# Kernel optimization log

Hardware: AMD Instinct MI355X
Metric: run time of the kernel (lower is better)

## Reference

```python
import jax, jax.numpy as jnp
import numpy as np

N = 262144          # total atoms
B = 2048            # graphs (batch.max()+1)
HID = 256           # hidden
CND = 128           # cond_proj_dim
K = 16              # n_clusters
PH = 8              # pool_heads
DH = HID // PH      # head_dim


def setup_inputs() -> dict:
    key = jax.random.key(0)
    ks = jax.random.split(key, 20)
    s = 0.02
    inp = {
        "h_atom": jax.random.normal(ks[0], (N, HID), jnp.float32),
        "c_atom": jax.random.normal(ks[1], (N, CND), jnp.float32),
        "batch": jnp.sort(jax.random.randint(ks[2], (N,), 0, B)).astype(jnp.int64),
        # gate: Linear(HID+CND, HID) -> GELU -> Linear(HID, 1) -> Sigmoid
        "W1": jax.random.normal(ks[3], (HID + CND, HID), jnp.float32) * s,
        "b1": jnp.zeros((HID,), jnp.float32),
        "W2": jax.random.normal(ks[4], (HID, 1), jnp.float32) * s,
        "b2": jnp.zeros((1,), jnp.float32),
        # assign: Linear(HID, HID) -> GELU -> Linear(HID, K)
        "A1": jax.random.normal(ks[5], (HID, HID), jnp.float32) * s,
        "ab1": jnp.zeros((HID,), jnp.float32),
        "A2": jax.random.normal(ks[6], (HID, K), jnp.float32) * s,
        "ab2": jnp.zeros((K,), jnp.float32),
        # cluster_proj: Linear(HID, HID)
        "Wc": jax.random.normal(ks[7], (HID, HID), jnp.float32) * s,
        "bc": jnp.zeros((HID,), jnp.float32),
        # readout
        "q": jax.random.normal(ks[8], (PH, DH), jnp.float32),   # readout_q param
        "Wk": jax.random.normal(ks[9], (HID, HID), jnp.float32) * s,
        "Wv": jax.random.normal(ks[10], (HID, HID), jnp.float32) * s,
        # LayerNorm
        "gamma": jnp.ones((HID,), jnp.float32),
        "beta": jnp.zeros((HID,), jnp.float32),
    }
    return inp


def reference(h_atom, c_atom, batch, W1, b1, W2, b2, A1, ab1, A2, ab2,
              Wc, bc, q, Wk, Wv, gamma, beta):
    gelu = lambda x: jax.nn.gelu(x, approximate=False)  # torch default GELU (erf)
    # Stage 1: condition-aware gating
    g = gelu(jnp.concatenate([h_atom, c_atom], axis=-1) @ W1 + b1)
    alpha = jax.nn.sigmoid(g @ W2 + b2)                 # [N, 1]
    h_gated = alpha * h_atom                            # [N, HID]
    # Stage 2: soft cluster assignment
    S = jax.nn.softmax(gelu(h_gated @ A1 + ab1) @ A2 + ab2, axis=-1)  # [N, K]
    # Ragged per-graph segment matmul: cluster[b,k,:] = sum_{n in graph b} S[n,k] * h_gated[n,:]
    cluster = jnp.stack(
        [jax.ops.segment_sum(h_gated * S[:, k:k + 1], batch, num_segments=B)
         for k in range(K)], axis=1)                    # [B, K, HID]
    cluster = cluster @ Wc + bc                         # cluster_proj
    # Stage 3: multi-head attention readout over K clusters
    Kp = (cluster @ Wk).reshape(B, K, PH, DH)
    Vp = (cluster @ Wv).reshape(B, K, PH, DH)
    scale = DH ** -0.5
    logits = jnp.einsum('pd,bkpd->bpk', q, Kp) * scale  # [B, PH, K]
    w = jax.nn.softmax(logits, axis=-1)                 # dropout p=0 -> identity
    out = jnp.einsum('bpk,bkpd->bpd', w, Vp).reshape(B, HID)
    # LayerNorm (eps = 1e-5, torch default)
    mu = out.mean(axis=-1, keepdims=True)
    var = ((out - mu) ** 2).mean(axis=-1, keepdims=True)
    return (out - mu) * jax.lax.rsqrt(var + 1e-5) * gamma + beta
```

## Files before the change

### kernel.cpp

```cpp
#include <hip/hip_runtime.h>
#include <hip/hip_bf16.h>
#include <math.h>
#include <stdint.h>

#define NATOMS 262144
#define BGRAPH 2048
#define CHUNK 10240

typedef __bf16 bf16_t;
typedef __bf16 bf16x8 __attribute__((ext_vector_type(8)));
typedef __bf16 bf16x4 __attribute__((ext_vector_type(4)));
typedef float f32x4 __attribute__((ext_vector_type(4)));

__device__ __forceinline__ float bf2f(bf16_t x){ return (float)x; }
__device__ __forceinline__ float gelu_f(float x){ return 0.5f*x*(1.0f+erff(x*0.70710678118654752f)); }

__device__ __forceinline__ void gl_lds16(const void* g, void* l){
    __attribute__((address_space(3))) uint32_t* lp =
        reinterpret_cast<__attribute__((address_space(3))) uint32_t*>(
            reinterpret_cast<uintptr_t>(l));
    __builtin_amdgcn_global_load_lds(static_cast<const uint32_t*>(g), lp, 16, 0, 0);
}

__global__ void bounds_kernel(const int* __restrict__ batch,
                              const unsigned* __restrict__ gamma,
                              int* __restrict__ starts, int* __restrict__ flags) {
    if (blockIdx.x == 0 && threadIdx.x == 0)
        flags[0] = (gamma[0] == 0x3F803F80u) ? 1 : 0;
    int b = blockIdx.x * 256 + threadIdx.x;
    if (b > BGRAPH) return;
    int is64 = (batch[NATOMS - 1] == 0) ? 1 : 0;
    int lo = 0, hi = NATOMS;
    while (lo < hi) {
        int mid = (lo + hi) >> 1;
        int v = is64 ? batch[2 * mid] : batch[mid];
        if (v < b) lo = mid + 1; else hi = mid;
    }
    starts[b] = lo;
}

__global__ void params_kernel(const void* b1, const void* W2, const void* ab1,
                              const void* bc, const void* q, const void* gamma,
                              const void* beta, const void* ab2, const void* b2,
                              float* __restrict__ P, const int* __restrict__ flags) {
    int t = threadIdx.x;
    int bf = flags[0];
#define CV(p,i) (bf ? bf2f(((const bf16_t*)(p))[i]) : ((const float*)(p))[i])
    P[t]        = CV(b1, t);
    P[256 + t]  = CV(W2, t);
    P[512 + t]  = CV(ab1, t);
    P[768 + t]  = CV(bc, t);
    P[1024 + t] = CV(q, t);
    P[1280 + t] = CV(gamma, t);
    P[1536 + t] = CV(beta, t);
    if (t < 16) P[1792 + t] = CV(ab2, t);
    if (t == 16) P[1808] = CV(b2, 0);
#undef CV
}

__global__ void chunk_transpose(const void* __restrict__ src, bf16_t* __restrict__ dst,
                                int Kd, int Nn, const int* __restrict__ flags) {
    int i = blockIdx.x * 256 + threadIdx.x;
    if (i >= Kd * Nn) return;
    int k = i / Nn, n = i - k * Nn;
    bf16_t v = flags[0] ? ((const bf16_t*)src)[i] : (bf16_t)(((const float*)src)[i]);
    dst[((size_t)(k >> 5) * Nn + n) * 40 + (k & 31)] = v;
}

__global__ void a2_transpose(const void* __restrict__ src, bf16_t* __restrict__ dst,
                             const int* __restrict__ flags) {
    int i = blockIdx.x * 256 + threadIdx.x;
    if (i >= 256 * 16) return;
    int k = i >> 4, n = i & 15;
    bf16_t v = flags[0] ? ((const bf16_t*)src)[i] : (bf16_t)(((const float*)src)[i]);
    dst[n * 256 + k] = v;
}

__global__ void c_convert(const float* __restrict__ c, bf16_t* __restrict__ cb,
                          const int* __restrict__ flags) {
    if (flags[0]) return;
    const size_t total = (size_t)NATOMS * 128 / 8;
    for (size_t i = (size_t)blockIdx.x * 256 + threadIdx.x; i < total; i += (size_t)2048 * 256) {
        const float4* s = (const float4*)c + i * 2;
        float4 a = s[0], b = s[1];
        bf16x8 v = { (bf16_t)a.x,(bf16_t)a.y,(bf16_t)a.z,(bf16_t)a.w,
                     (bf16_t)b.x,(bf16_t)b.y,(bf16_t)b.z,(bf16_t)b.w };
        *(bf16x8*)(cb + i * 8) = v;
    }
}

__global__ __launch_bounds__(256, 2) void atom_kernel(
    const void* __restrict__ h, const void* __restrict__ cnd, const bf16_t* __restrict__ cb,
    const bf16_t* __restrict__ W1c, const bf16_t* __restrict__ A1c,
    const bf16_t* __restrict__ A2t, const float* __restrict__ P,
    const int* __restrict__ flags,
    bf16_t* __restrict__ hg_out, float* __restrict__ S_out)
{
    __shared__ bf16_t ldsX[64 * 264];
    __shared__ bf16_t ldsW[2][CHUNK];
    __shared__ float  ldsV[256];
    __shared__ float  ldsB1[256];
    __shared__ float  ldsAB1[256];
    __shared__ float  ldsAlpha[64];

    const int tid  = threadIdx.x;
    const int wave = tid >> 6;
    const int lane = tid & 63;
    const int quad = lane >> 4;
    const int l15  = lane & 15;
    const int a0   = blockIdx.x * 64;
    const int dbf  = flags[0];

    const bf16_t* cbp = dbf ? (const bf16_t*)cnd : cb;

    bf16x8 cf[4][4];
#pragma unroll
    for (int kc = 0; kc < 4; ++kc)
#pragma unroll
        for (int mt = 0; mt < 4; ++mt)
            cf[kc][mt] = *(const bf16x8*)(cbp + (size_t)(a0 + mt * 16 + l15) * 128 + kc * 32 + quad * 8);

    ldsV[tid]   = P[256 + tid];
    ldsB1[tid]  = P[tid];
    ldsAB1[tid] = P[512 + tid];
    if (tid < 64) ldsAlpha[tid] = 0.f;
    const float b2v = P[1808];

    if (dbf) {
        const uint4* hs = (const uint4*)((const bf16_t*)h + (size_t)a0 * 256);
#pragma unroll
        for (int i = 0; i < 8; ++i) {
            int lin = i * 256 + tid; int row = lin >> 5; int off = lin & 31;
            *(uint4*)(&ldsX[row * 264 + off * 8]) = hs[row * 32 + off];
        }
    } else {
        const float4* hs = (const float4*)((const float*)h + (size_t)a0 * 256);
#pragma unroll
        for (int i = 0; i < 16; ++i) {
            int lin = i * 256 + tid; int row = lin >> 6; int off = lin & 63;
            float4 v = hs[row * 64 + off];
            bf16x4 w = { (bf16_t)v.x, (bf16_t)v.y, (bf16_t)v.z, (bf16_t)v.w };
            *(bf16x4*)(&ldsX[row * 264 + off * 4]) = w;
        }
    }

    auto stage = [&](int bsel, const bf16_t* src){
#pragma unroll
        for (int i = 0; i < 5; ++i) {
            int u = i * 256 + wave * 64;
            gl_lds16(src + (size_t)(u + lane) * 8, &ldsW[bsel][u * 8]);
        }
    };

    stage(0, W1c);
    __syncthreads();

    f32x4 acc[4][4];
#pragma unroll
    for (int a = 0; a < 4; ++a)
#pragma unroll
        for (int b = 0; b < 4; ++b) acc[a][b] = (f32x4){0.f,0.f,0.f,0.f};

#pragma unroll
    for (int ks = 0; ks < 12; ++ks) {
        const int cur = ks & 1;
        const bf16_t* nxt = (ks < 11) ? (W1c + (size_t)(ks + 1) * CHUNK) : A1c;
        stage(cur ^ 1, nxt);
        bf16x8 af[4], bv[4];
#pragma unroll
        for (int j = 0; j < 4; ++j)
            bv[j] = *(const bf16x8*)(&ldsW[cur][(wave * 64 + j * 16 + l15) * 40 + quad * 8]);
        if (ks < 8) {
            int kb = ks * 32 + quad * 8;
#pragma unroll
            for (int mt = 0; mt < 4; ++mt) af[mt] = *(const bf16x8*)(&ldsX[(mt * 16 + l15) * 264 + kb]);
        } else {
#pragma unroll
            for (int mt = 0; mt < 4; ++mt) af[mt] = cf[ks - 8][mt];
        }
        __builtin_amdgcn_s_setprio(1);
#pragma unroll
        for (int mt = 0; mt < 4; ++mt)
#pragma unroll
            for (int j = 0; j < 4; ++j)
                acc[mt][j] = __builtin_amdgcn_mfma_f32_16x16x32_bf16(af[mt], bv[j], acc[mt][j], 0, 0, 0);
        __builtin_amdgcn_s_setprio(0);
        __syncthreads();
    }

    for (int mt = 0; mt < 4; ++mt) {
        float p[4] = {0.f, 0.f, 0.f, 0.f};
        for (int j = 0; j < 4; ++j) {
            int col = wave * 64 + j * 16 + l15;
            float w = ldsV[col];
            float bb = ldsB1[col];
            for (int r = 0; r < 4; ++r) {
                float g = gelu_f(acc[mt][j][r] + bb);
                p[r] += g * w;
            }
        }
        for (int off = 1; off < 16; off <<= 1)
            for (int r = 0; r < 4; ++r) p[r] += __shfl_xor(p[r], off, 64);
        if (l15 == 0)
            for (int r = 0; r < 4; ++r)
                atomicAdd(&ldsAlpha[mt * 16 + quad * 4 + r], p[r]);
    }
    __syncthreads();

    {
        int r = tid >> 2, p4 = tid & 3;
        float al = 1.f / (1.f + expf(-(ldsAlpha[r] + b2v)));
        bf16_t* xrow = &ldsX[r * 264 + p4 * 64];
        bf16_t* grow = hg_out + (size_t)(a0 + r) * 256 + p4 * 64;
        for (int i = 0; i < 8; ++i) {
            bf16x8 v = *(bf16x8*)(xrow + i * 8);
            for (int e = 0; e < 8; ++e) v[e] = (bf16_t)(bf2f(v[e]) * al);
            *(bf16x8*)(xrow + i * 8) = v;
            *(bf16x8*)(grow + i * 8) = v;
        }
    }
    __syncthreads();

#pragma unroll
    for (int a = 0; a < 4; ++a)
#pragma unroll
        for (int b = 0; b < 4; ++b) acc[a][b] = (f32x4){0.f,0.f,0.f,0.f};
#pragma unroll
    for (int ks = 0; ks < 8; ++ks) {
        const int cur = ks & 1;
        if (ks < 7) stage(cur ^ 1, A1c + (size_t)(ks + 1) * CHUNK);
        bf16x8 af[4], bv[4];
        int kb = ks * 32 + quad * 8;
#pragma unroll
        for (int j = 0; j < 4; ++j)
            bv[j] = *(const bf16x8*)(&ldsW[cur][(wave * 64 + j * 16 + l15) * 40 + quad * 8]);
#pragma unroll
        for (int mt = 0; mt < 4; ++mt) af[mt] = *(const bf16x8*)(&ldsX[(mt * 16 + l15) * 264 + kb]);
        __builtin_amdgcn_s_setprio(1);
#pragma unroll
        for (int mt = 0; mt < 4; ++mt)
#pragma unroll
            for (int j = 0; j < 4; ++j)
                acc[mt][j] = __builtin_amdgcn_mfma_f32_16x16x32_bf16(af[mt], bv[j], acc[mt][j], 0, 0, 0);
        __builtin_amdgcn_s_setprio(0);
        __syncthreads();
    }

    for (int mt = 0; mt < 4; ++mt)
        for (int j = 0; j < 4; ++j) {
            int col = wave * 64 + j * 16 + l15;
            float bb = ldsAB1[col];
            for (int r = 0; r < 4; ++r) {
                int row = mt * 16 + quad * 4 + r;
                ldsX[row * 264 + col] = (bf16_t)gelu_f(acc[mt][j][r] + bb);
            }
        }
    if (tid < 128) {
        int n = tid >> 3, k0 = (tid & 7) * 32;
#pragma unroll
        for (int p = 0; p < 4; ++p)
            *(uint4*)(&ldsW[0][n * 264 + k0 + p * 8]) = *(const uint4*)(A2t + n * 256 + k0 + p * 8);
    }
    __syncthreads();

    f32x4 acc3 = (f32x4){0.f,0.f,0.f,0.f};
#pragma unroll
    for (int ks = 0; ks < 8; ++ks) {
        int kb = ks * 32 + quad * 8;
        bf16x8 a = *(const bf16x8*)(&ldsX[(wave * 16 + l15) * 264 + kb]);
        bf16x8 b = *(const bf16x8*)(&ldsW[0][l15 * 264 + kb]);
        acc3 = __builtin_amdgcn_mfma_f32_16x16x32_bf16(a, b, acc3, 0, 0, 0);
    }
    float ab2v = P[1792 + l15];
    float lv[4], mx[4], ex[4], sm[4];
    for (int r = 0; r < 4; ++r) { lv[r] = acc3[r] + ab2v; mx[r] = lv[r]; }
    for (int off = 1; off < 16; off <<= 1)
        for (int r = 0; r < 4; ++r) { float o = __shfl_xor(mx[r], off, 64); mx[r] = fmaxf(mx[r], o); }
    for (int r = 0; r < 4; ++r) { ex[r] = expf(lv[r] - mx[r]); sm[r] = ex[r]; }
    for (int off = 1; off < 16; off <<= 1)
        for (int r = 0; r < 4; ++r) sm[r] += __shfl_xor(sm[r], off, 64);
    for (int r = 0; r < 4; ++r) {
        int row = wave * 16 + quad * 4 + r;
        S_out[(size_t)(a0 + row) * 16 + l15] = ex[r] / sm[r];
    }
}

__global__ __launch_bounds__(256) void segment_kernel(
    const bf16_t* __restrict__ hg, const float* __restrict__ S,
    const int* __restrict__ starts, bf16_t* __restrict__ craw)
{
    __shared__ float ldsS[16 * 16];
    int b = blockIdx.x, tid = threadIdx.x;
    int s = starts[b], e = starts[b + 1];
    float acc[16];
#pragma unroll
    for (int k = 0; k < 16; ++k) acc[k] = 0.f;
    for (int n0 = s; n0 < e; n0 += 16) {
        int cnt = min(16, e - n0);
        if (tid < cnt * 16) ldsS[tid] = S[(size_t)(n0 + (tid >> 4)) * 16 + (tid & 15)];
        __syncthreads();
        for (int a = 0; a < cnt; ++a) {
            float v = bf2f(hg[(size_t)(n0 + a) * 256 + tid]);
            const f32x4* sr = (const f32x4*)(&ldsS[a * 16]);
            f32x4 s0 = sr[0], s1 = sr[1], s2 = sr[2], s3 = sr[3];
            acc[0]  += s0[0] * v; acc[1]  += s0[1] * v; acc[2]  += s0[2] * v; acc[3]  += s0[3] * v;
            acc[4]  += s1[0] * v; acc[5]  += s1[1] * v; acc[6]  += s1[2] * v; acc[7]  += s1[3] * v;
            acc[8]  += s2[0] * v; acc[9]  += s2[1] * v; acc[10] += s2[2] * v; acc[11] += s2[3] * v;
            acc[12] += s3[0] * v; acc[13] += s3[1] * v; acc[14] += s3[2] * v; acc[15] += s3[3] * v;
        }
        __syncthreads();
    }
#pragma unroll
    for (int k = 0; k < 16; ++k)
        craw[((size_t)b * 16 + k) * 256 + tid] = (bf16_t)acc[k];
}

__global__ __launch_bounds__(256, 2) void gemm_kernel(
    const bf16_t* __restrict__ A, const bf16_t* __restrict__ Wck,
    const float* __restrict__ bias, bf16_t* __restrict__ C)
{
    __shared__ bf16_t ldsA[64 * 264];
    __shared__ bf16_t ldsW[2][CHUNK];
    const int tid = threadIdx.x;
    const int wave = tid >> 6, lane = tid & 63, quad = lane >> 4, l15 = lane & 15;
    const size_t r0 = (size_t)blockIdx.x * 64;

    auto stage = [&](int bsel, const bf16_t* src){
#pragma unroll
        for (int i = 0; i < 5; ++i) {
            int u = i * 256 + wave * 64;
            gl_lds16(src + (size_t)(u + lane) * 8, &ldsW[bsel][u * 8]);
        }
    };

    const uint4* as = (const uint4*)(A + r0 * 256);
#pragma unroll
    for (int i = 0; i < 8; ++i) {
        int lin = i * 256 + tid; int row = lin >> 5; int off = lin & 31;
        *(uint4*)(&ldsA[row * 264 + off * 8]) = as[row * 32 + off];
    }
    stage(0, Wck);
    __syncthreads();

    f32x4 acc[4][4];
#pragma unroll
    for (int a = 0; a < 4; ++a)
#pragma unroll
        for (int b = 0; b < 4; ++b) acc[a][b] = (f32x4){0.f,0.f,0.f,0.f};

#pragma unroll
    for (int ks = 0; ks < 8; ++ks) {
        const int cur = ks & 1;
        if (ks < 7) stage(cur ^ 1, Wck + (size_t)(ks + 1) * CHUNK);
        bf16x8 af[4], bv[4];
        int kb = ks * 32 + quad * 8;
#pragma unroll
        for (int j = 0; j < 4; ++j)
            bv[j] = *(const bf16x8*)(&ldsW[cur][(wave * 64 + j * 16 + l15) * 40 + quad * 8]);
#pragma unroll
        for (int mt = 0; mt < 4; ++mt) af[mt] = *(const bf16x8*)(&ldsA[(mt * 16 + l15) * 264 + kb]);
        __builtin_amdgcn_s_setprio(1);
#pragma unroll
        for (int mt = 0; mt < 4; ++mt)
#pragma unroll
            for (int j = 0; j < 4; ++j)
                acc[mt][j] = __builtin_amdgcn_mfma_f32_16x16x32_bf16(af[mt], bv[j], acc[mt][j], 0, 0, 0);
        __builtin_amdgcn_s_setprio(0);
        __syncthreads();
    }
    for (int mt = 0; mt < 4; ++mt)
        for (int j = 0; j < 4; ++j) {
            int col = wave * 64 + j * 16 + l15;
            float bvl = bias ? bias[col] : 0.f;
            for (int r = 0; r < 4; ++r)
                C[(r0 + mt * 16 + quad * 4 + r) * 256 + col] = (bf16_t)(acc[mt][j][r] + bvl);
        }
}

__global__ __launch_bounds__(256, 2) void gemm2x_kernel(
    const bf16_t* __restrict__ A, const bf16_t* __restrict__ Wkc, const bf16_t* __restrict__ Wvc,
    bf16_t* __restrict__ CK, bf16_t* __restrict__ CV)
{
    __shared__ bf16_t ldsA[64 * 264];
    __shared__ bf16_t ldsW[2][CHUNK];
    const int tid = threadIdx.x;
    const int wave = tid >> 6, lane = tid & 63, quad = lane >> 4, l15 = lane & 15;
    const size_t r0 = (size_t)blockIdx.x * 64;

    auto stage = [&](int bsel, const bf16_t* src){
#pragma unroll
        for (int i = 0; i < 5; ++i) {
            int u = i * 256 + wave * 64;
            gl_lds16(src + (size_t)(u + lane) * 8, &ldsW[bsel][u * 8]);
        }
    };

    const uint4* as = (const uint4*)(A + r0 * 256);
#pragma unroll
    for (int i = 0; i < 8; ++i) {
        int lin = i * 256 + tid; int row = lin >> 5; int off = lin & 31;
        *(uint4*)(&ldsA[row * 264 + off * 8]) = as[row * 32 + off];
    }
    stage(0, Wkc);
    __syncthreads();

    f32x4 acc[4][4];
#pragma unroll
    for (int a = 0; a < 4; ++a)
#pragma unroll
        for (int b = 0; b < 4; ++b) acc[a][b] = (f32x4){0.f,0.f,0.f,0.f};

#pragma unroll
    for (int ks = 0; ks < 8; ++ks) {
        const int cur = ks & 1;
        const bf16_t* nxt = (ks < 7) ? (Wkc + (size_t)(ks + 1) * CHUNK) : Wvc;
        stage(cur ^ 1, nxt);
        bf16x8 af[4], bv[4];
        int kb = ks * 32 + quad * 8;
#pragma unroll
        for (int j = 0; j < 4; ++j)
            bv[j] = *(const bf16x8*)(&ldsW[cur][(wave * 64 + j * 16 + l15) * 40 + quad * 8]);
#pragma unroll
        for (int mt = 0; mt < 4; ++mt) af[mt] = *(const bf16x8*)(&ldsA[(mt * 16 + l15) * 264 + kb]);
        __builtin_amdgcn_s_setprio(1);
#pragma unroll
        for (int mt = 0; mt < 4; ++mt)
#pragma unroll
            for (int j = 0; j < 4; ++j)
                acc[mt][j] = __builtin_amdgcn_mfma_f32_16x16x32_bf16(af[mt], bv[j], acc[mt][j], 0, 0, 0);
        __builtin_amdgcn_s_setprio(0);
        __syncthreads();
    }
    for (int mt = 0; mt < 4; ++mt)
        for (int j = 0; j < 4; ++j) {
            int col = wave * 64 + j * 16 + l15;
            for (int r = 0; r < 4; ++r)
                CK[(r0 + mt * 16 + quad * 4 + r) * 256 + col] = (bf16_t)acc[mt][j][r];
        }

#pragma unroll
    for (int a = 0; a < 4; ++a)
#pragma unroll
        for (int b = 0; b < 4; ++b) acc[a][b] = (f32x4){0.f,0.f,0.f,0.f};
#pragma unroll
    for (int ks = 0; ks < 8; ++ks) {
        const int cur = ks & 1;
        if (ks < 7) stage(cur ^ 1, Wvc + (size_t)(ks + 1) * CHUNK);
        bf16x8 af[4], bv[4];
        int kb = ks * 32 + quad * 8;
#pragma unroll
        for (int j = 0; j < 4; ++j)
            bv[j] = *(const bf16x8*)(&ldsW[cur][(wave * 64 + j * 16 + l15) * 40 + quad * 8]);
#pragma unroll
        for (int mt = 0; mt < 4; ++mt) af[mt] = *(const bf16x8*)(&ldsA[(mt * 16 + l15) * 264 + kb]);
        __builtin_amdgcn_s_setprio(1);
#pragma unroll
        for (int mt = 0; mt < 4; ++mt)
#pragma unroll
            for (int j = 0; j < 4; ++j)
                acc[mt][j] = __builtin_amdgcn_mfma_f32_16x16x32_bf16(af[mt], bv[j], acc[mt][j], 0, 0, 0);
        __builtin_amdgcn_s_setprio(0);
        __syncthreads();
    }
    for (int mt = 0; mt < 4; ++mt)
        for (int j = 0; j < 4; ++j) {
            int col = wave * 64 + j * 16 + l15;
            for (int r = 0; r < 4; ++r)
                CV[(r0 + mt * 16 + quad * 4 + r) * 256 + col] = (bf16_t)acc[mt][j][r];
        }
}

__global__ __launch_bounds__(256) void attn_ln_kernel(
    const bf16_t* __restrict__ Kp, const bf16_t* __restrict__ Vp,
    const float* __restrict__ P, const int* __restrict__ flags,
    void* __restrict__ out)
{
    __shared__ float lw[8][16];
    __shared__ float w1s[4], w2s[4];
    int b = blockIdx.x, tid = threadIdx.x;
    const int dbf = flags[0];
    const float* q     = P + 1024;
    const float* gamma = P + 1280;
    const float* beta  = P + 1536;
    if (tid < 128) {
        int p = tid >> 4, k = tid & 15;
        const bf16x8* kr = (const bf16x8*)(Kp + ((size_t)b * 16 + k) * 256 + p * 32);
        const float* qr = q + p * 32;
        float dot = 0.f;
#pragma unroll
        for (int i = 0; i < 4; ++i) {
            bf16x8 v = kr[i];
#pragma unroll
            for (int e = 0; e < 8; ++e) dot += qr[i * 8 + e] * bf2f(v[e]);
        }
        lw[p][k] = dot * 0.17677669529663687f;
    }
    __syncthreads();
    if (tid < 8) {
        float m = -1e30f;
        for (int k = 0; k < 16; ++k) m = fmaxf(m, lw[tid][k]);
        float s = 0.f;
        for (int k = 0; k < 16; ++k) { float ev = expf(lw[tid][k] - m); lw[tid][k] = ev; s += ev; }
        float inv = 1.f / s;
        for (int k = 0; k < 16; ++k) lw[tid][k] *= inv;
    }
    __syncthreads();
    int p = tid >> 5, d = tid & 31;
    float o = 0.f;
    for (int k = 0; k < 16; ++k)
        o += lw[p][k] * bf2f(Vp[((size_t)b * 16 + k) * 256 + p * 32 + d]);
    float s1 = o, s2 = o * o;
    for (int off = 1; off < 64; off <<= 1) { s1 += __shfl_xor(s1, off, 64); s2 += __shfl_xor(s2, off, 64); }
    int wv = tid >> 6;
    if ((tid & 63) == 0) { w1s[wv] = s1; w2s[wv] = s2; }
    __syncthreads();
    float ts1 = w1s[0] + w1s[1] + w1s[2] + w1s[3];
    float ts2 = w2s[0] + w2s[1] + w2s[2] + w2s[3];
    float mu = ts1 * (1.f / 256.f);
    float var = ts2 * (1.f / 256.f) - mu * mu;
    float y = (o - mu) * rsqrtf(var + 1e-5f) * gamma[tid] + beta[tid];
    if (dbf) ((bf16_t*)out)[(size_t)b * 256 + tid] = (bf16_t)y;
    else     ((float*)out)[(size_t)b * 256 + tid]  = y;
}

extern "C" void kernel_launch(void* const* d_in, const int* in_sizes, int n_in,
                              void* d_out, int out_size, void* d_ws, size_t ws_size,
                              hipStream_t stream) {
    const void* h     = d_in[0];
    const void* cnd   = d_in[1];
    const int*  batch = (const int*)d_in[2];
    const void* W1    = d_in[3];
    const void* b1    = d_in[4];
    const void* W2    = d_in[5];
    const void* b2    = d_in[6];
    const void* A1    = d_in[7];
    const void* ab1   = d_in[8];
    const void* A2    = d_in[9];
    const void* ab2   = d_in[10];
    const void* Wc    = d_in[11];
    const void* bc    = d_in[12];
    const void* q     = d_in[13];
    const void* Wk    = d_in[14];
    const void* Wv    = d_in[15];
    const void* gamma = d_in[16];
    const void* beta  = d_in[17];

    char* ws = (char*)d_ws;
    size_t off = 0;
    bf16_t* W1c  = (bf16_t*)(ws + off); off += 12 * CHUNK * 2;
    bf16_t* A1c  = (bf16_t*)(ws + off); off += 8 * CHUNK * 2;
    bf16_t* Wcc  = (bf16_t*)(ws + off); off += 8 * CHUNK * 2;
    bf16_t* Wkc  = (bf16_t*)(ws + off); off += 8 * CHUNK * 2;
    bf16_t* Wvc  = (bf16_t*)(ws + off); off += 8 * CHUNK * 2;
    bf16_t* A2t  = (bf16_t*)(ws + off); off += 8192;
    float*  P    = (float*)(ws + off);  off += 8192;
    int*    flags = (int*)(ws + off);   off += 256;
    int*    starts = (int*)(ws + off);  off += 8448;
    float*  S    = (float*)(ws + off);  off += (size_t)NATOMS * 16 * 4;
    bf16_t* hg   = (bf16_t*)(ws + off); off += (size_t)NATOMS * 256 * 2;
    bf16_t* craw = (bf16_t*)(ws + off); off += (size_t)BGRAPH * 16 * 256 * 2;
    bf16_t* cP   = (bf16_t*)(ws + off); off += (size_t)BGRAPH * 16 * 256 * 2;
    bf16_t* KpB  = (bf16_t*)(ws + off); off += (size_t)BGRAPH * 16 * 256 * 2;
    bf16_t* VpB  = (bf16_t*)(ws + off); off += (size_t)BGRAPH * 16 * 256 * 2;
    bf16_t* cb   = craw;
    (void)ws_size; (void)n_in; (void)in_sizes; (void)out_size;

    bounds_kernel<<<9, 256, 0, stream>>>(batch, (const unsigned*)gamma, starts, flags);
    params_kernel<<<1, 256, 0, stream>>>(b1, W2, ab1, bc, q, gamma, beta, ab2, b2, P, flags);
    chunk_transpose<<<(384 * 256 + 255) / 256, 256, 0, stream>>>(W1, W1c, 384, 256, flags);
    chunk_transpose<<<(256 * 256 + 255) / 256, 256, 0, stream>>>(A1, A1c, 256, 256, flags);
    chunk_transpose<<<(256 * 256 + 255) / 256, 256, 0, stream>>>(Wc, Wcc, 256, 256, flags);
    chunk_transpose<<<(256 * 256 + 255) / 256, 256, 0, stream>>>(Wk, Wkc, 256, 256, flags);
    chunk_transpose<<<(256 * 256 + 255) / 256, 256, 0, stream>>>(Wv, Wvc, 256, 256, flags);
    a2_transpose<<<16, 256, 0, stream>>>(A2, A2t, flags);
    c_convert<<<2048, 256, 0, stream>>>((const float*)cnd, cb, flags);

    atom_kernel<<<NATOMS / 64, 256, 0, stream>>>(h, cnd, cb, W1c, A1c, A2t, P, flags, hg, S);
    segment_kernel<<<BGRAPH, 256, 0, stream>>>(hg, S, starts, craw);
    gemm_kernel<<<BGRAPH * 16 / 64, 256, 0, stream>>>(craw, Wcc, P + 768, cP);
    gemm2x_kernel<<<BGRAPH * 16 / 64, 256, 0, stream>>>(cP, Wkc, Wvc, KpB, VpB);
    attn_ln_kernel<<<BGRAPH, 256, 0, stream>>>(KpB, VpB, P, flags, d_out);
}
```

Before: 835.9 us.

## Merge prep kernels, fuse cluster GEMMs, enlarge atom tiles, use fast GELU/exp

Nine small setup launches are merged into one prep kernel that dispatches on block index. The cluster_proj GEMM and the K/V GEMM are fused, so the projected cluster stays in LDS instead of round-tripping through global memory. The atom kernel now runs 128 atoms per 512-thread block with 64-wide K steps, which halves the barrier count per unit of work and shares weight staging across twice as many rows, but it roughly doubles LDS per block and may lower occupancy. erf in GELU is replaced by the Abramowitz-Stegun polynomial, and exp and reciprocal use fast intrinsics, trading a little accuracy for fewer instructions.

Measured after the change: 807.6 us. 3.4% less time.

```diff
diff --git a/kernel.cpp b/kernel.cpp
--- a/kernel.cpp
+++ b/kernel.cpp
@@ -13,7 +13,17 @@
 typedef float f32x4 __attribute__((ext_vector_type(4)));
 
 __device__ __forceinline__ float bf2f(bf16_t x){ return (float)x; }
-__device__ __forceinline__ float gelu_f(float x){ return 0.5f*x*(1.0f+erff(x*0.70710678118654752f)); }
+
+__device__ __forceinline__ float gelu_f(float x){
+    float s  = x * 0.70710678118654752f;
+    float a  = fabsf(s);
+    float t  = __builtin_amdgcn_rcpf(fmaf(0.3275911f, a, 1.0f));
+    float p  = t * fmaf(t, fmaf(t, fmaf(t, fmaf(t, 1.061405429f, -1.453152027f),
+                                        1.421413741f), -0.284496736f), 0.254829592f);
+    float e  = __expf(-a * a);
+    float er = copysignf(fmaf(-p, e, 1.0f), s);
+    return 0.5f * x * (1.0f + er);
+}
 
 __device__ __forceinline__ void gl_lds16(const void* g, void* l){
     __attribute__((address_space(3))) uint32_t* lp =
@@ -22,93 +32,113 @@
     __builtin_amdgcn_global_load_lds(static_cast<const uint32_t*>(g), lp, 16, 0, 0);
 }
 
-__global__ void bounds_kernel(const int* __restrict__ batch,
-                              const unsigned* __restrict__ gamma,
-                              int* __restrict__ starts, int* __restrict__ flags) {
-    if (blockIdx.x == 0 && threadIdx.x == 0)
-        flags[0] = (gamma[0] == 0x3F803F80u) ? 1 : 0;
-    int b = blockIdx.x * 256 + threadIdx.x;
-    if (b > BGRAPH) return;
-    int is64 = (batch[NATOMS - 1] == 0) ? 1 : 0;
-    int lo = 0, hi = NATOMS;
-    while (lo < hi) {
-        int mid = (lo + hi) >> 1;
-        int v = is64 ? batch[2 * mid] : batch[mid];
-        if (v < b) lo = mid + 1; else hi = mid;
-    }
-    starts[b] = lo;
-}
-
-__global__ void params_kernel(const void* b1, const void* W2, const void* ab1,
-                              const void* bc, const void* q, const void* gamma,
-                              const void* beta, const void* ab2, const void* b2,
-                              float* __restrict__ P, const int* __restrict__ flags) {
-    int t = threadIdx.x;
-    int bf = flags[0];
+#define PREP_W1 10
+#define PREP_A1 394
+#define PREP_WC 650
+#define PREP_WK 906
+#define PREP_WV 1162
+#define PREP_A2 1418
+#define PREP_C  1434
+#define PREP_END 3482
+
+__device__ __forceinline__ void chunk_tr(const void* src, bf16_t* dst, int Kd, int idx, int bf){
+    if (idx >= Kd * 256) return;
+    int k = idx >> 8, n = idx & 255;
+    bf16_t v = bf ? ((const bf16_t*)src)[idx] : (bf16_t)(((const float*)src)[idx]);
+    dst[((size_t)(k >> 5) * 256 + n) * 40 + (k & 31)] = v;
+}
+
+__global__ void prep_kernel(
+    const int* __restrict__ batch, const void* __restrict__ gamma,
+    const void* b1, const void* W2, const void* ab1, const void* bc,
+    const void* q, const void* beta, const void* ab2, const void* b2,
+    const void* W1, const void* A1, const void* Wc, const void* Wk, const void* Wv,
+    const void* A2, const void* cnd,
+    bf16_t* __restrict__ W1c, bf16_t* __restrict__ A1c, bf16_t* __restrict__ Wcc,
+    bf16_t* __restrict__ Wkc, bf16_t* __restrict__ Wvc, bf16_t* __restrict__ A2t,
+    float* __restrict__ P, int* __restrict__ flags, int* __restrict__ starts,
+    bf16_t* __restrict__ cbOut)
+{
+    const int tid = threadIdx.x, blk = blockIdx.x;
+    const int bf = (((const unsigned*)gamma)[0] == 0x3F803F80u) ? 1 : 0;
+    if (blk == 0 && tid == 0) flags[0] = bf;
+
+    if (blk < 9) {
+        int b = blk * 256 + tid;
+        if (b > BGRAPH) return;
+        int is64 = (batch[NATOMS - 1] == 0) ? 1 : 0;
+        int lo = 0, hi = NATOMS;
+        while (lo < hi) {
+            int mid = (lo + hi) >> 1;
+            int v = is64 ? batch[2 * mid] : batch[mid];
+            if (v < b) lo = mid + 1; else hi = mid;
+        }
+        starts[b] = lo;
+        return;
+    }
+    if (blk == 9) {
 #define CV(p,i) (bf ? bf2f(((const bf16_t*)(p))[i]) : ((const float*)(p))[i])
-    P[t]        = CV(b1, t);
-    P[256 + t]  = CV(W2, t);
-    P[512 + t]  = CV(ab1, t);
-    P[768 + t]  = CV(bc, t);
-    P[1024 + t] = CV(q, t);
-    P[1280 + t] = CV(gamma, t);
-    P[1536 + t] = CV(beta, t);
-    if (t < 16) P[1792 + t] = CV(ab2, t);
-    if (t == 16) P[1808] = CV(b2, 0);
+        P[tid]        = CV(b1, tid);
+        P[256 + tid]  = CV(W2, tid);
+        P[512 + tid]  = CV(ab1, tid);
+        P[768 + tid]  = CV(bc, tid);
+        P[1024 + tid] = CV(q, tid);
+        P[1280 + tid] = CV(gamma, tid);
+        P[1536 + tid] = CV(beta, tid);
+        if (tid < 16) P[1792 + tid] = CV(ab2, tid);
+        if (tid == 16) P[1808] = CV(b2, 0);
 #undef CV
-}
-
-__global__ void chunk_transpose(const void* __restrict__ src, bf16_t* __restrict__ dst,
-                                int Kd, int Nn, const int* __restrict__ flags) {
-    int i = blockIdx.x * 256 + threadIdx.x;
-    if (i >= Kd * Nn) return;
-    int k = i / Nn, n = i - k * Nn;
-    bf16_t v = flags[0] ? ((const bf16_t*)src)[i] : (bf16_t)(((const float*)src)[i]);
-    dst[((size_t)(k >> 5) * Nn + n) * 40 + (k & 31)] = v;
-}
-
-__global__ void a2_transpose(const void* __restrict__ src, bf16_t* __restrict__ dst,
-                             const int* __restrict__ flags) {
-    int i = blockIdx.x * 256 + threadIdx.x;
-    if (i >= 256 * 16) return;
-    int k = i >> 4, n = i & 15;
-    bf16_t v = flags[0] ? ((const bf16_t*)src)[i] : (bf16_t)(((const float*)src)[i]);
-    dst[n * 256 + k] = v;
-}
-
-__global__ void c_convert(const float* __restrict__ c, bf16_t* __restrict__ cb,
-                          const int* __restrict__ flags) {
-    if (flags[0]) return;
+        return;
+    }
+    if (blk < PREP_A1) { chunk_tr(W1, W1c, 384, (blk - PREP_W1) * 256 + tid, bf); return; }
+    if (blk < PREP_WC) { chunk_tr(A1, A1c, 256, (blk - PREP_A1) * 256 + tid, bf); return; }
+    if (blk < PREP_WK) { chunk_tr(Wc, Wcc, 256, (blk - PREP_WC) * 256 + tid, bf); return; }
+    if (blk < PREP_WV) { chunk_tr(Wk, Wkc, 256, (blk - PREP_WK) * 256 + tid, bf); return; }
+    if (blk < PREP_A2) { chunk_tr(Wv, Wvc, 256, (blk - PREP_WV) * 256 + tid, bf); return; }
+    if (blk < PREP_C)  {
+        int i = (blk - PREP_A2) * 256 + tid;
+        if (i >= 256 * 16) return;
+        int k = i >> 4, n = i & 15;
+        bf16_t v = bf ? ((const bf16_t*)A2)[i] : (bf16_t)(((const float*)A2)[i]);
+        A2t[n * 256 + k] = v;
+        return;
+    }
+    if (bf) return;
+    size_t i = (size_t)(blk - PREP_C) * 256 + tid;
     const size_t total = (size_t)NATOMS * 128 / 8;
-    for (size_t i = (size_t)blockIdx.x * 256 + threadIdx.x; i < total; i += (size_t)2048 * 256) {
-        const float4* s = (const float4*)c + i * 2;
+#pragma unroll
+    for (int it = 0; it < 8; ++it, i += 524288) {
+        if (i >= total) break;
+        const float4* s = (const float4*)cnd + i * 2;
         float4 a = s[0], b = s[1];
         bf16x8 v = { (bf16_t)a.x,(bf16_t)a.y,(bf16_t)a.z,(bf16_t)a.w,
                      (bf16_t)b.x,(bf16_t)b.y,(bf16_t)b.z,(bf16_t)b.w };
-        *(bf16x8*)(cb + i * 8) = v;
-    }
-}
-
-__global__ __launch_bounds__(256, 2) void atom_kernel(
+        *(bf16x8*)(cbOut + i * 8) = v;
+    }
+}
+
+__global__ __launch_bounds__(512, 2) void atom_kernel(
     const void* __restrict__ h, const void* __restrict__ cnd, const bf16_t* __restrict__ cb,
     const bf16_t* __restrict__ W1c, const bf16_t* __restrict__ A1c,
     const bf16_t* __restrict__ A2t, const float* __restrict__ P,
     const int* __restrict__ flags,
     bf16_t* __restrict__ hg_out, float* __restrict__ S_out)
 {
-    __shared__ bf16_t ldsX[64 * 264];
-    __shared__ bf16_t ldsW[2][CHUNK];
+    __shared__ bf16_t ldsX[128 * 264];
+    __shared__ bf16_t ldsW[2][2 * CHUNK];
     __shared__ float  ldsV[256];
     __shared__ float  ldsB1[256];
     __shared__ float  ldsAB1[256];
-    __shared__ float  ldsAlpha[64];
+    __shared__ float  ldsAlpha[128];
 
     const int tid  = threadIdx.x;
     const int wave = tid >> 6;
     const int lane = tid & 63;
     const int quad = lane >> 4;
     const int l15  = lane & 15;
-    const int a0   = blockIdx.x * 64;
+    const int wr   = wave >> 2;
+    const int wc   = wave & 3;
+    const int a0   = blockIdx.x * 128;
     const int dbf  = flags[0];
 
     const bf16_t* cbp = dbf ? (const bf16_t*)cnd : cb;
@@ -118,26 +148,24 @@
     for (int kc = 0; kc < 4; ++kc)
 #pragma unroll
         for (int mt = 0; mt < 4; ++mt)
-            cf[kc][mt] = *(const bf16x8*)(cbp + (size_t)(a0 + mt * 16 + l15) * 128 + kc * 32 + quad * 8);
-
-    ldsV[tid]   = P[256 + tid];
-    ldsB1[tid]  = P[tid];
-    ldsAB1[tid] = P[512 + tid];
-    if (tid < 64) ldsAlpha[tid] = 0.f;
+            cf[kc][mt] = *(const bf16x8*)(cbp + (size_t)(a0 + wr * 64 + mt * 16 + l15) * 128 + kc * 32 + quad * 8);
+
+    if (tid < 256) { ldsV[tid] = P[256 + tid]; ldsB1[tid] = P[tid]; ldsAB1[tid] = P[512 + tid]; }
+    if (tid < 128) ldsAlpha[tid] = 0.f;
     const float b2v = P[1808];
 
     if (dbf) {
         const uint4* hs = (const uint4*)((const bf16_t*)h + (size_t)a0 * 256);
 #pragma unroll
         for (int i = 0; i < 8; ++i) {
-            int lin = i * 256 + tid; int row = lin >> 5; int off = lin & 31;
+            int lin = i * 512 + tid; int row = lin >> 5; int off = lin & 31;
             *(uint4*)(&ldsX[row * 264 + off * 8]) = hs[row * 32 + off];
         }
     } else {
         const float4* hs = (const float4*)((const float*)h + (size_t)a0 * 256);
 #pragma unroll
         for (int i = 0; i < 16; ++i) {
-            int lin = i * 256 + tid; int row = lin >> 6; int off = lin & 63;
+            int lin = i * 512 + tid; int row = lin >> 6; int off = lin & 63;
             float4 v = hs[row * 64 + off];
             bf16x4 w = { (bf16_t)v.x, (bf16_t)v.y, (bf16_t)v.z, (bf16_t)v.w };
             *(bf16x4*)(&ldsX[row * 264 + off * 4]) = w;
@@ -147,8 +175,8 @@
     auto stage = [&](int bsel, const bf16_t* src){
 #pragma unroll
         for (int i = 0; i < 5; ++i) {
-            int u = i * 256 + wave * 64;
-            gl_lds16(src + (size_t)(u + lane) * 8, &ldsW[bsel][u * 8]);
+            int u = i * 512 + wave * 64;
+            gl_lds16(src + (size_t)(u + lane) * 8, &ldsW[bsel][0] + (size_t)u * 8);
         }
     };
 
@@ -162,28 +190,37 @@
         for (int b = 0; b < 4; ++b) acc[a][b] = (f32x4){0.f,0.f,0.f,0.f};
 
 #pragma unroll
-    for (int ks = 0; ks < 12; ++ks) {
+    for (int ks = 0; ks < 6; ++ks) {
         const int cur = ks & 1;
-        const bf16_t* nxt = (ks < 11) ? (W1c + (size_t)(ks + 1) * CHUNK) : A1c;
+        const bf16_t* nxt = (ks < 5) ? (W1c + (size_t)(ks + 1) * 2 * CHUNK) : A1c;
         stage(cur ^ 1, nxt);
-        bf16x8 af[4], bv[4];
-#pragma unroll
-        for (int j = 0; j < 4; ++j)
-            bv[j] = *(const bf16x8*)(&ldsW[cur][(wave * 64 + j * 16 + l15) * 40 + quad * 8]);
-        if (ks < 8) {
-            int kb = ks * 32 + quad * 8;
-#pragma unroll
-            for (int mt = 0; mt < 4; ++mt) af[mt] = *(const bf16x8*)(&ldsX[(mt * 16 + l15) * 264 + kb]);
+        bf16x8 af[2][4], bv[2][4];
+#pragma unroll
+        for (int kh = 0; kh < 2; ++kh)
+#pragma unroll
+            for (int j = 0; j < 4; ++j)
+                bv[kh][j] = *(const bf16x8*)(&ldsW[cur][kh * CHUNK + (wc * 64 + j * 16 + l15) * 40 + quad * 8]);
+        if (ks < 4) {
+#pragma unroll
+            for (int kh = 0; kh < 2; ++kh)
+#pragma unroll
+                for (int mt = 0; mt < 4; ++mt)
+                    af[kh][mt] = *(const bf16x8*)(&ldsX[(wr * 64 + mt * 16 + l15) * 264 + ks * 64 + kh * 32 + quad * 8]);
         } else {
 #pragma unroll
-            for (int mt = 0; mt < 4; ++mt) af[mt] = cf[ks - 8][mt];
+            for (int kh = 0; kh < 2; ++kh)
+#pragma unroll
+                for (int mt = 0; mt < 4; ++mt)
+                    af[kh][mt] = cf[(ks - 4) * 2 + kh][mt];
         }
         __builtin_amdgcn_s_setprio(1);
 #pragma unroll
-        for (int mt = 0; mt < 4; ++mt)
-#pragma unroll
-            for (int j = 0; j < 4; ++j)
-                acc[mt][j] = __builtin_amdgcn_mfma_f32_16x16x32_bf16(af[mt], bv[j], acc[mt][j], 0, 0, 0);
+        for (int kh = 0; kh < 2; ++kh)
+#pragma unroll
+            for (int mt = 0; mt < 4; ++mt)
+#pragma unroll
+                for (int j = 0; j < 4; ++j)
+                    acc[mt][j] = __builtin_amdgcn_mfma_f32_16x16x32_bf16(af[kh][mt], bv[kh][j], acc[mt][j], 0, 0, 0);
         __builtin_amdgcn_s_setprio(0);
         __syncthreads();
     }
@@ -191,7 +228,7 @@
     for (int mt = 0; mt < 4; ++mt) {
         float p[4] = {0.f, 0.f, 0.f, 0.f};
         for (int j = 0; j < 4; ++j) {
-            int col = wave * 64 + j * 16 + l15;
+            int col = wc * 64 + j * 16 + l15;
             float w = ldsV[col];
             float bb = ldsB1[col];
             for (int r = 0; r < 4; ++r) {
@@ -203,13 +240,13 @@
             for (int r = 0; r < 4; ++r) p[r] += __shfl_xor(p[r], off, 64);
         if (l15 == 0)
             for (int r = 0; r < 4; ++r)
-                atomicAdd(&ldsAlpha[mt * 16 + quad * 4 + r], p[r]);
+                atomicAdd(&ldsAlpha[wr * 64 + mt * 16 + quad * 4 + r], p[r]);
     }
     __syncthreads();
 
     {
         int r = tid >> 2, p4 = tid & 3;
-        float al = 1.f / (1.f + expf(-(ldsAlpha[r] + b2v)));
+        float al = __builtin_amdgcn_rcpf(1.f + __expf(-(ldsAlpha[r] + b2v)));
         bf16_t* xrow = &ldsX[r * 264 + p4 * 64];
         bf16_t* grow = hg_out + (size_t)(a0 + r) * 256 + p4 * 64;
         for (int i = 0; i < 8; ++i) {
@@ -226,32 +263,37 @@
 #pragma unroll
         for (int b = 0; b < 4; ++b) acc[a][b] = (f32x4){0.f,0.f,0.f,0.f};
 #pragma unroll
-    for (int ks = 0; ks < 8; ++ks) {
+    for (int ks = 0; ks < 4; ++ks) {
         const int cur = ks & 1;
-        if (ks < 7) stage(cur ^ 1, A1c + (size_t)(ks + 1) * CHUNK);
-        bf16x8 af[4], bv[4];
-        int kb = ks * 32 + quad * 8;
-#pragma unroll
-        for (int j = 0; j < 4; ++j)
-            bv[j] = *(const bf16x8*)(&ldsW[cur][(wave * 64 + j * 16 + l15) * 40 + quad * 8]);
-#pragma unroll
-        for (int mt = 0; mt < 4; ++mt) af[mt] = *(const bf16x8*)(&ldsX[(mt * 16 + l15) * 264 + kb]);
+        if (ks < 3) stage(cur ^ 1, A1c + (size_t)(ks + 1) * 2 * CHUNK);
+        bf16x8 af[2][4], bv[2][4];
+#pragma unroll
+        for (int kh = 0; kh < 2; ++kh) {
+#pragma unroll
+            for (int j = 0; j < 4; ++j)
+                bv[kh][j] = *(const bf16x8*)(&ldsW[cur][kh * CHUNK + (wc * 64 + j * 16 + l15) * 40 + quad * 8]);
+#pragma unroll
+            for (int mt = 0; mt < 4; ++mt)
+                af[kh][mt] = *(const bf16x8*)(&ldsX[(wr * 64 + mt * 16 + l15) * 264 + ks * 64 + kh * 32 + quad * 8]);
+        }
         __builtin_amdgcn_s_setprio(1);
 #pragma unroll
-        for (int mt = 0; mt < 4; ++mt)
-#pragma unroll
-            for (int j = 0; j < 4; ++j)
-                acc[mt][j] = __builtin_amdgcn_mfma_f32_16x16x32_bf16(af[mt], bv[j], acc[mt][j], 0, 0, 0);
+        for (int kh = 0; kh < 2; ++kh)
+#pragma unroll
+            for (int mt = 0; mt < 4; ++mt)
+#pragma unroll
+                for (int j = 0; j < 4; ++j)
+                    acc[mt][j] = __builtin_amdgcn_mfma_f32_16x16x32_bf16(af[kh][mt], bv[kh][j], acc[mt][j], 0, 0, 0);
         __builtin_amdgcn_s_setprio(0);
         __syncthreads();
     }
 
     for (int mt = 0; mt < 4; ++mt)
         for (int j = 0; j < 4; ++j) {
-            int col = wave * 64 + j * 16 + l15;
+            int col = wc * 64 + j * 16 + l15;
             float bb = ldsAB1[col];
             for (int r = 0; r < 4; ++r) {
-                int row = mt * 16 + quad * 4 + r;
+                int row = wr * 64 + mt * 16 + quad * 4 + r;
                 ldsX[row * 264 + col] = (bf16_t)gelu_f(acc[mt][j][r] + bb);
             }
         }
@@ -276,7 +318,7 @@
     for (int r = 0; r < 4; ++r) { lv[r] = acc3[r] + ab2v; mx[r] = lv[r]; }
     for (int off = 1; off < 16; off <<= 1)
         for (int r = 0; r < 4; ++r) { float o = __shfl_xor(mx[r], off, 64); mx[r] = fmaxf(mx[r], o); }
-    for (int r = 0; r < 4; ++r) { ex[r] = expf(lv[r] - mx[r]); sm[r] = ex[r]; }
+    for (int r = 0; r < 4; ++r) { ex[r] = __expf(lv[r] - mx[r]); sm[r] = ex[r]; }
     for (int off = 1; off < 16; off <<= 1)
         for (int r = 0; r < 4; ++r) sm[r] += __shfl_xor(sm[r], off, 64);
     for (int r = 0; r < 4; ++r) {
@@ -315,70 +357,10 @@
         craw[((size_t)b * 16 + k) * 256 + tid] = (bf16_t)acc[k];
 }
 
-__global__ __launch_bounds__(256, 2) void gemm_kernel(
-    const bf16_t* __restrict__ A, const bf16_t* __restrict__ Wck,
-    const float* __restrict__ bias, bf16_t* __restrict__ C)
-{
-    __shared__ bf16_t ldsA[64 * 264];
-    __shared__ bf16_t ldsW[2][CHUNK];
-    const int tid = threadIdx.x;
-    const int wave = tid >> 6, lane = tid & 63, quad = lane >> 4, l15 = lane & 15;
-    const size_t r0 = (size_t)blockIdx.x * 64;
-
-    auto stage = [&](int bsel, const bf16_t* src){
-#pragma unroll
-        for (int i = 0; i < 5; ++i) {
-            int u = i * 256 + wave * 64;
-            gl_lds16(src + (size_t)(u + lane) * 8, &ldsW[bsel][u * 8]);
-        }
-    };
-
-    const uint4* as = (const uint4*)(A + r0 * 256);
-#pragma unroll
-    for (int i = 0; i < 8; ++i) {
-        int lin = i * 256 + tid; int row = lin >> 5; int off = lin & 31;
-        *(uint4*)(&ldsA[row * 264 + off * 8]) = as[row * 32 + off];
-    }
-    stage(0, Wck);
-    __syncthreads();
-
-    f32x4 acc[4][4];
-#pragma unroll
-    for (int a = 0; a < 4; ++a)
-#pragma unroll
-        for (int b = 0; b < 4; ++b) acc[a][b] = (f32x4){0.f,0.f,0.f,0.f};
-
-#pragma unroll
-    for (int ks = 0; ks < 8; ++ks) {
-        const int cur = ks & 1;
-        if (ks < 7) stage(cur ^ 1, Wck + (size_t)(ks + 1) * CHUNK);
-        bf16x8 af[4], bv[4];
-        int kb = ks * 32 + quad * 8;
-#pragma unroll
-        for (int j = 0; j < 4; ++j)
-            bv[j] = *(const bf16x8*)(&ldsW[cur][(wave * 64 + j * 16 + l15) * 40 + quad * 8]);
-#pragma unroll
-        for (int mt = 0; mt < 4; ++mt) af[mt] = *(const bf16x8*)(&ldsA[(mt * 16 + l15) * 264 + kb]);
-        __builtin_amdgcn_s_setprio(1);
-#pragma unroll
-        for (int mt = 0; mt < 4; ++mt)
-#pragma unroll
-            for (int j = 0; j < 4; ++j)
-                acc[mt][j] = __builtin_amdgcn_mfma_f32_16x16x32_bf16(af[mt], bv[j], acc[mt][j], 0, 0, 0);
-        __builtin_amdgcn_s_setprio(0);
-        __syncthreads();
-    }
-    for (int mt = 0; mt < 4; ++mt)
-        for (int j = 0; j < 4; ++j) {
-            int col = wave * 64 + j * 16 + l15;
-            float bvl = bias ? bias[col] : 0.f;
-            for (int r = 0; r < 4; ++r)
-                C[(r0 + mt * 16 + quad * 4 + r) * 256 + col] = (bf16_t)(acc[mt][j][r] + bvl);
-        }
-}
-
-__global__ __launch_bounds__(256, 2) void gemm2x_kernel(
-    const bf16_t* __restrict__ A, const bf16_t* __restrict__ Wkc, const bf16_t* __restrict__ Wvc,
+__global__ __launch_bounds__(256, 2) void cluster_kernel(
+    const bf16_t* __restrict__ A, const bf16_t* __restrict__ Wcc,
+    const bf16_t* __restrict__ Wkc, const bf16_t* __restrict__ Wvc,
+    const float* __restrict__ P,
     bf16_t* __restrict__ CK, bf16_t* __restrict__ CV)
 {
     __shared__ bf16_t ldsA[64 * 264];
@@ -386,12 +368,13 @@
     const int tid = threadIdx.x;
     const int wave = tid >> 6, lane = tid & 63, quad = lane >> 4, l15 = lane & 15;
     const size_t r0 = (size_t)blockIdx.x * 64;
+    const float* bias = P + 768;
 
     auto stage = [&](int bsel, const bf16_t* src){
 #pragma unroll
         for (int i = 0; i < 5; ++i) {
             int u = i * 256 + wave * 64;
-            gl_lds16(src + (size_t)(u + lane) * 8, &ldsW[bsel][u * 8]);
+            gl_lds16(src + (size_t)(u + lane) * 8, &ldsW[bsel][0] + (size_t)u * 8);
         }
     };
 
@@ -401,15 +384,49 @@
         int lin = i * 256 + tid; int row = lin >> 5; int off = lin & 31;
         *(uint4*)(&ldsA[row * 264 + off * 8]) = as[row * 32 + off];
     }
-    stage(0, Wkc);
+    stage(0, Wcc);
     __syncthreads();
 
     f32x4 acc[4][4];
+
 #pragma unroll
     for (int a = 0; a < 4; ++a)
 #pragma unroll
         for (int b = 0; b < 4; ++b) acc[a][b] = (f32x4){0.f,0.f,0.f,0.f};
-
+#pragma unroll
+    for (int ks = 0; ks < 8; ++ks) {
+        const int cur = ks & 1;
+        const bf16_t* nxt = (ks < 7) ? (Wcc + (size_t)(ks + 1) * CHUNK) : Wkc;
+        stage(cur ^ 1, nxt);
+        bf16x8 af[4], bv[4];
+        int kb = ks * 32 + quad * 8;
+#pragma unroll
+        for (int j = 0; j < 4; ++j)
+            bv[j] = *(const bf16x8*)(&ldsW[cur][(wave * 64 + j * 16 + l15) * 40 + quad * 8]);
+#pragma unroll
+        for (int mt = 0; mt < 4; ++mt) af[mt] = *(const bf16x8*)(&ldsA[(mt * 16 + l15) * 264 + kb]);
+        __builtin_amdgcn_s_setprio(1);
+#pragma unroll
+        for (int mt = 0; mt < 4; ++mt)
+#pragma unroll
+            for (int j = 0; j < 4; ++j)
+                acc[mt][j] = __builtin_amdgcn_mfma_f32_16x16x32_bf16(af[mt], bv[j], acc[mt][j], 0, 0, 0);
+        __builtin_amdgcn_s_setprio(0);
+        __syncthreads();
+    }
+    for (int mt = 0; mt < 4; ++mt)
+        for (int j = 0; j < 4; ++j) {
+            int col = wave * 64 + j * 16 + l15;
+            float bvl = bias[col];
+            for (int r = 0; r < 4; ++r)
+                ldsA[(mt * 16 + quad * 4 + r) * 264 + col] = (bf16_t)(acc[mt][j][r] + bvl);
+        }
+    __syncthreads();
+
+#pragma unroll
+    for (int a = 0; a < 4; ++a)
+#pragma unroll
+        for (int b = 0; b < 4; ++b) acc[a][b] = (f32x4){0.f,0.f,0.f,0.f};
 #pragma unroll
     for (int ks = 0; ks < 8; ++ks) {
         const int cur = ks & 1;
@@ -500,7 +517,7 @@
         float m = -1e30f;
         for (int k = 0; k < 16; ++k) m = fmaxf(m, lw[tid][k]);
         float s = 0.f;
-        for (int k = 0; k < 16; ++k) { float ev = expf(lw[tid][k] - m); lw[tid][k] = ev; s += ev; }
+        for (int k = 0; k < 16; ++k) { float ev = __expf(lw[tid][k] - m); lw[tid][k] = ev; s += ev; }
         float inv = 1.f / s;
         for (int k = 0; k < 16; ++k) lw[tid][k] *= inv;
     }
@@ -559,25 +576,19 @@
     float*  S    = (float*)(ws + off);  off += (size_t)NATOMS * 16 * 4;
     bf16_t* hg   = (bf16_t*)(ws + off); off += (size_t)NATOMS * 256 * 2;
     bf16_t* craw = (bf16_t*)(ws + off); off += (size_t)BGRAPH * 16 * 256 * 2;
-    bf16_t* cP   = (bf16_t*)(ws + off); off += (size_t)BGRAPH * 16 * 256 * 2;
+    bf16_t* padA = (bf16_t*)(ws + off); off += (size_t)BGRAPH * 16 * 256 * 2;
     bf16_t* KpB  = (bf16_t*)(ws + off); off += (size_t)BGRAPH * 16 * 256 * 2;
     bf16_t* VpB  = (bf16_t*)(ws + off); off += (size_t)BGRAPH * 16 * 256 * 2;
     bf16_t* cb   = craw;
-    (void)ws_size; (void)n_in; (void)in_sizes; (void)out_size;
-
-    bounds_kernel<<<9, 256, 0, stream>>>(batch, (const unsigned*)gamma, starts, flags);
-    params_kernel<<<1, 256, 0, stream>>>(b1, W2, ab1, bc, q, gamma, beta, ab2, b2, P, flags);
-    chunk_transpose<<<(384 * 256 + 255) / 256, 256, 0, stream>>>(W1, W1c, 384, 256, flags);
-    chunk_transpose<<<(256 * 256 + 255) / 256, 256, 0, stream>>>(A1, A1c, 256, 256, flags);
-    chunk_transpose<<<(256 * 256 + 255) / 256, 256, 0, stream>>>(Wc, Wcc, 256, 256, flags);
-    chunk_transpose<<<(256 * 256 + 255) / 256, 256, 0, stream>>>(Wk, Wkc, 256, 256, flags);
-    chunk_transpose<<<(256 * 256 + 255) / 256, 256, 0, stream>>>(Wv, Wvc, 256, 256, flags);
-    a2_transpose<<<16, 256, 0, stream>>>(A2, A2t, flags);
-    c_convert<<<2048, 256, 0, stream>>>((const float*)cnd, cb, flags);
-
-    atom_kernel<<<NATOMS / 64, 256, 0, stream>>>(h, cnd, cb, W1c, A1c, A2t, P, flags, hg, S);
+    (void)padA; (void)ws_size; (void)n_in; (void)in_sizes; (void)out_size;
+
+    prep_kernel<<<PREP_END, 256, 0, stream>>>(
+        batch, gamma, b1, W2, ab1, bc, q, beta, ab2, b2,
+        W1, A1, Wc, Wk, Wv, A2, cnd,
+        W1c, A1c, Wcc, Wkc, Wvc, A2t, P, flags, starts, cb);
+
+    atom_kernel<<<NATOMS / 128, 512, 0, stream>>>(h, cnd, cb, W1c, A1c, A2t, P, flags, hg, S);
     segment_kernel<<<BGRAPH, 256, 0, stream>>>(hg, S, starts, craw);
-    gemm_kernel<<<BGRAPH * 16 / 64, 256, 0, stream>>>(craw, Wcc, P + 768, cP);
-    gemm2x_kernel<<<BGRAPH * 16 / 64, 256, 0, stream>>>(cP, Wkc, Wvc, KpB, VpB);
+    cluster_kernel<<<BGRAPH * 16 / 64, 256, 0, stream>>>(craw, Wcc, Wkc, Wvc, P, KpB, VpB);
     attn_ln_kernel<<<BGRAPH, 256, 0, stream>>>(KpB, VpB, P, flags, d_out);
 }
```
